# Kernel tuning notes

Hardware: AMD Instinct MI355X
Metric: run time of the kernel (lower is better)

## Reference

```python
import jax, jax.numpy as jnp
import numpy as np

N_NODES = 100000
N_EDGES = 1600000
IN_DIM, HID_DIM, OUT_DIM = 128, 128, 64


def setup_inputs() -> dict:
    key = jax.random.key(0)
    k1, k2, k3, k4 = jax.random.split(key, 4)
    x = jax.random.normal(k1, (N_NODES, IN_DIM), dtype=jnp.float32)
    edge_index = jax.random.randint(k2, (2, N_EDGES), 0, N_NODES, dtype=jnp.int64)
    W1 = jax.random.normal(k3, (IN_DIM, HID_DIM), dtype=jnp.float32) * (1.0 / np.sqrt(IN_DIM))
    b1 = jnp.zeros((HID_DIM,), dtype=jnp.float32)
    W2 = jax.random.normal(k4, (HID_DIM, OUT_DIM), dtype=jnp.float32) * (1.0 / np.sqrt(HID_DIM))
    b2 = jnp.zeros((OUT_DIM,), dtype=jnp.float32)
    return {"x": x, "edge_index": edge_index, "W1": W1, "b1": b1, "W2": W2, "b2": b2}


def _gcn_conv(h, src, dst, norm, W, b, n_nodes):
    # Dense transform first (PyG GCNConv order), then gather-scatter aggregation.
    h = h @ W                                   # [N, out]
    msg = h[src] * norm[:, None]                # [E, out] gather + scale
    out = jax.ops.segment_sum(msg, dst, num_segments=n_nodes)  # scatter-add
    return out + b


def reference(x, edge_index, W1, b1, W2, b2):
    src, dst = edge_index[0], edge_index[1]
    n = x.shape[0]
    # symmetric normalization: deg from in-degree (unit edge weights), no self loops
    deg = jax.ops.segment_sum(jnp.ones_like(src, dtype=x.dtype), dst, num_segments=n)
    deg_inv_sqrt = jnp.where(deg > 0, jax.lax.rsqrt(jnp.maximum(deg, 1.0)), 0.0)
    norm = deg_inv_sqrt[src] * deg_inv_sqrt[dst]  # [E]
    h = jax.nn.relu(_gcn_conv(x, src, dst, norm, W1, b1, n))
    # dropout is identity in eval mode
    out = _gcn_conv(h, src, dst, norm, W2, b2, n)
    return out
```

## Files before the change

kernel.cpp:

```cpp
#include <hip/hip_runtime.h>
#include <stdint.h>

#define NN 100000
#define NE 1600000
#define K_DIM 128

#define BSH 7
#define NBKT ((NN + (1 << BSH) - 1) >> BSH)
#define EPT 32
#define BIN_CHUNK (256 * EPT)
#define CAP 4096
#define PADE 2400000

typedef unsigned int uint32;
typedef unsigned short ushort16;
typedef __attribute__((ext_vector_type(8))) short bf16x8;
typedef __attribute__((ext_vector_type(4))) float f32x4;

__device__ __forceinline__ ushort16 f2bf(float f) {
    uint32 u = __float_as_uint(f);
    u += 0x7fffu + ((u >> 16) & 1u);
    return (ushort16)(u >> 16);
}
__device__ __forceinline__ float bf_lo(uint32 u) { return __uint_as_float(u << 16); }
__device__ __forceinline__ float bf_hi(uint32 u) { return __uint_as_float(u & 0xffff0000u); }

#define ACC8(v) do { \
    a0 += bf_lo((v).x); a1 += bf_hi((v).x); \
    a2 += bf_lo((v).y); a3 += bf_hi((v).y); \
    a4 += bf_lo((v).z); a5 += bf_hi((v).z); \
    a6 += bf_lo((v).w); a7 += bf_hi((v).w); } while (0)

__device__ __forceinline__ bf16x8 ld_frag8(const ushort16* p) {
    uint2 lo = *(const uint2*)p;
    uint2 hi = *(const uint2*)(p + 4);
    union { uint32 u[4]; bf16x8 v; } x;
    x.u[0] = lo.x; x.u[1] = lo.y; x.u[2] = hi.x; x.u[3] = hi.y;
    return x.v;
}


__global__ __launch_bounds__(256) void bin_pass1_kernel(
        const int* __restrict__ ei, int* __restrict__ gcursor,
        uint2* __restrict__ staging) {
    __shared__ int hist[NBKT];
    __shared__ int base[NBKT];
    int tid = threadIdx.x;
    int e0 = blockIdx.x * BIN_CHUNK;

    for (int i = tid; i < NBKT; i += 256) hist[i] = 0;
    __syncthreads();

    #pragma unroll
    for (int k = 0; k < EPT; k++) {
        int e = e0 + k * 256 + tid;
        if (e < NE) {
            int d = ei[NE + e];
            atomicAdd(&hist[d >> BSH], 1);
        }
    }
    __syncthreads();

    for (int i = tid; i < NBKT; i += 256) {
        int c = hist[i];
        base[i] = c ? atomicAdd(&gcursor[i], c) : 0;
        hist[i] = 0;
    }
    __syncthreads();

    #pragma unroll
    for (int k = 0; k < EPT; k++) {
        int e = e0 + k * 256 + tid;
        if (e < NE) {
            int s = ei[e];
            int d = ei[NE + e];
            int b = d >> BSH;
            int off = atomicAdd(&hist[b], 1);
            staging[(size_t)b * CAP + base[b] + off] = make_uint2((uint32)s, (uint32)d);
        }
    }
}

__global__ __launch_bounds__(256) void deg_bucket_kernel(
        const uint2* __restrict__ staging, const int* __restrict__ gcursor,
        int* __restrict__ deg, float* __restrict__ dis, int* __restrict__ bucket_tot) {
    __shared__ int cnt[1 << BSH];
    __shared__ int red[1 << BSH];
    int b = blockIdx.x;
    int node0 = b << BSH;
    int tid = threadIdx.x;
    int n_edges = gcursor[b];

    if (tid < (1 << BSH)) cnt[tid] = 0;
    __syncthreads();

    for (int i = tid; i < n_edges; i += 256) {
        uint2 p = staging[(size_t)b * CAP + i];
        atomicAdd(&cnt[p.y & ((1 << BSH) - 1)], 1);
    }
    __syncthreads();

    if (tid < (1 << BSH)) {
        int node = node0 + tid;
        int c = cnt[tid];
        if (node < NN) {
            deg[node] = c;
            dis[node] = (c > 0) ? rsqrtf((float)c) : 0.0f;
            red[tid] = (c + 7) & ~7;
        } else {
            red[tid] = 0;
        }
    }
    __syncthreads();
    for (int off = (1 << BSH) / 2; off > 0; off >>= 1) {
        if (tid < off) red[tid] += red[tid + off];
        __syncthreads();
    }
    if (tid == 0) bucket_tot[b] = red[0];
}

__global__ void bucket_scan_kernel(const int* __restrict__ bucket_tot,
                                   int* __restrict__ bucket_base,
                                   int* __restrict__ row_start) {
    __shared__ int buf[1024];
    int tid = threadIdx.x;
    int v = (tid < NBKT) ? bucket_tot[tid] : 0;
    buf[tid] = v;
    __syncthreads();
    for (int off = 1; off < 1024; off <<= 1) {
        int t = (tid >= off) ? buf[tid - off] : 0;
        __syncthreads();
        buf[tid] += t;
        __syncthreads();
    }
    if (tid < NBKT) bucket_base[tid] = buf[tid] - v;
    if (tid == NBKT - 1) row_start[NN] = buf[tid];
}

__global__ __launch_bounds__(256) void bin_pass2_kernel(
        const uint2* __restrict__ staging, const int* __restrict__ gcursor,
        const int* __restrict__ deg, const int* __restrict__ bucket_base,
        int* __restrict__ row_start, int* __restrict__ ssrc) {
    __shared__ int sb[1 << BSH];
    __shared__ int cur[1 << BSH];
    __shared__ int pend[1 << BSH];
    int b = blockIdx.x;
    int node0 = b << BSH;
    int tid = threadIdx.x;
    int n_edges = gcursor[b];

    int p = 0;
    if (tid < (1 << BSH)) {
        int node = node0 + tid;
        p = (node < NN) ? ((deg[node] + 7) & ~7) : 0;
        sb[tid] = p;
    }
    __syncthreads();
    #pragma unroll
    for (int off = 1; off < (1 << BSH); off <<= 1) {
        int t = (tid >= off && tid < (1 << BSH)) ? sb[tid - off] : 0;
        __syncthreads();
        if (tid < (1 << BSH)) sb[tid] += t;
        __syncthreads();
    }
    if (tid < (1 << BSH)) {
        int rs = bucket_base[b] + sb[tid] - p;
        cur[tid] = rs;
        pend[tid] = rs + p;
        int node = node0 + tid;
        if (node < NN) row_start[node] = rs;
    }
    __syncthreads();

    for (int i = tid; i < n_edges; i += 256) {
        uint2 pr = staging[(size_t)b * CAP + i];
        int off = atomicAdd(&cur[pr.y & ((1 << BSH) - 1)], 1);
        ssrc[off] = (int)pr.x;
    }
    __syncthreads();

    if (tid < (1 << BSH)) {
        int node = node0 + tid;
        if (node < NN) {
            for (int q = cur[tid]; q < pend[tid]; q++) ssrc[q] = NN;
        }
    }
}

template <int N, bool ABF16>
__global__ __launch_bounds__(256) void gemm_mfma_kernel(
        const void* __restrict__ Ap, const float* __restrict__ W,
        const float* __restrict__ dis, ushort16* __restrict__ out, int M) {
    constexpr int BM = 64, K = K_DIM;
    constexpr int LDA = 132;
    constexpr int NT = N / 16;
    constexpr int NLOG = (N == 128) ? 7 : 6;

    __shared__ ushort16 As[BM * LDA];
    __shared__ ushort16 Bt[N * LDA];

    int tid = threadIdx.x;
    int row0 = blockIdx.x * BM;

    if constexpr (!ABF16) {
        const float* A = (const float*)Ap;
        #pragma unroll
        for (int c = 0; c < 8; c++) {
            int idx = c * 1024 + tid * 4;
            int r = idx >> 7, col = idx & 127;
            int ra = row0 + r;
            float4 v = (ra < M) ? *(const float4*)&A[(size_t)ra * K + col]
                                : make_float4(0.f, 0.f, 0.f, 0.f);
            ushort4 bq;
            bq.x = f2bf(v.x); bq.y = f2bf(v.y); bq.z = f2bf(v.z); bq.w = f2bf(v.w);
            *(ushort4*)&As[r * LDA + col] = bq;
        }
    } else {
        const ushort16* A = (const ushort16*)Ap;
        #pragma unroll
        for (int c = 0; c < 4; c++) {
            int idx = c * 2048 + tid * 8;
            int r = idx >> 7, col = idx & 127;
            int ra = row0 + r;
            uint4 v = make_uint4(0u, 0u, 0u, 0u);
            if (ra < M) v = *(const uint4*)&A[(size_t)ra * K + col];
            *(uint2*)&As[r * LDA + col]     = make_uint2(v.x, v.y);
            *(uint2*)&As[r * LDA + col + 4] = make_uint2(v.z, v.w);
        }
    }
    {
        #pragma unroll
        for (int c = 0; c < (K * N) / 1024; c++) {
            int idx = c * 1024 + tid * 4;
            int k = idx >> NLOG, n = idx & (N - 1);
            float4 v = *(const float4*)&W[idx];
            Bt[(n + 0) * LDA + k] = f2bf(v.x);
            Bt[(n + 1) * LDA + k] = f2bf(v.y);
            Bt[(n + 2) * LDA + k] = f2bf(v.z);
            Bt[(n + 3) * LDA + k] = f2bf(v.w);
        }
    }
    __syncthreads();

    int lane = tid & 63;
    int wv = tid >> 6;
    int m0 = wv * 16;
    int ml = lane & 15;
    int quad = lane >> 4;

    f32x4 acc[NT];
    #pragma unroll
    for (int i = 0; i < NT; i++) acc[i] = (f32x4){0.f, 0.f, 0.f, 0.f};

    #pragma unroll
    for (int ks = 0; ks < 4; ks++) {
        int kof = ks * 32 + quad * 8;
        bf16x8 a = ld_frag8(&As[(m0 + ml) * LDA + kof]);
        #pragma unroll
        for (int nt = 0; nt < NT; nt++) {
            bf16x8 bb = ld_frag8(&Bt[(nt * 16 + ml) * LDA + kof]);
            acc[nt] = __builtin_amdgcn_mfma_f32_16x16x32_bf16(a, bb, acc[nt], 0, 0, 0);
        }
    }

    #pragma unroll
    for (int r = 0; r < 4; r++) {
        int row = row0 + m0 + quad * 4 + r;
        if (row < M) {
            float s = dis[row];
            #pragma unroll
            for (int nt = 0; nt < NT; nt++)
                out[(size_t)row * N + nt * 16 + ml] = f2bf(acc[nt][r] * s);
        }
    }
}

__global__ __launch_bounds__(256) void agg128_kernel(
        const ushort16* __restrict__ g, const int* __restrict__ row_start,
        const int* __restrict__ ssrc, const float* __restrict__ dis,
        const float* __restrict__ bias, ushort16* __restrict__ out) {
    int wave = (blockIdx.x * 256 + threadIdx.x) >> 6;
    int lane = threadIdx.x & 63;
    if (wave >= NN) return;

    int beg = row_start[wave];
    int end = row_start[wave + 1];
    int ecount = end - beg;
    float sc = dis[wave];

    int fl = lane & 15;
    int q  = lane >> 4;
    int laneoff = fl * 16;

    int idx = ssrc[beg + lane];

    float a0 = 0.f, a1 = 0.f, a2 = 0.f, a3 = 0.f;
    float a4 = 0.f, a5 = 0.f, a6 = 0.f, a7 = 0.f;

    const char* gb = (const char*)g;
    int nb = ((ecount < 64) ? ecount : 64) >> 3;
    int b = 0;
    for (; b + 2 <= nb; b += 2) {
        int s0a = __shfl(idx, b * 8 + q);
        int s1a = __shfl(idx, b * 8 + 4 + q);
        int s0b = __shfl(idx, b * 8 + 8 + q);
        int s1b = __shfl(idx, b * 8 + 12 + q);
        uint4 v0a = *(const uint4*)(gb + (((uint32)s0a << 8) + laneoff));
        uint4 v1a = *(const uint4*)(gb + (((uint32)s1a << 8) + laneoff));
        uint4 v0b = *(const uint4*)(gb + (((uint32)s0b << 8) + laneoff));
        uint4 v1b = *(const uint4*)(gb + (((uint32)s1b << 8) + laneoff));
        ACC8(v0a); ACC8(v1a); ACC8(v0b); ACC8(v1b);
    }
    if (b < nb) {
        int s0 = __shfl(idx, b * 8 + q);
        int s1 = __shfl(idx, b * 8 + 4 + q);
        uint4 v0 = *(const uint4*)(gb + (((uint32)s0 << 8) + laneoff));
        uint4 v1 = *(const uint4*)(gb + (((uint32)s1 << 8) + laneoff));
        ACC8(v0); ACC8(v1);
    }
    for (int e = beg + 64; e < end; e += 8) {
        int idx2 = ssrc[e + (lane & 7)];
        int s0 = __shfl(idx2, q);
        int s1 = __shfl(idx2, 4 + q);
        uint4 v0 = *(const uint4*)(gb + (((uint32)s0 << 8) + laneoff));
        uint4 v1 = *(const uint4*)(gb + (((uint32)s1 << 8) + laneoff));
        ACC8(v0); ACC8(v1);
    }

    a0 += __shfl_xor(a0, 16); a1 += __shfl_xor(a1, 16);
    a2 += __shfl_xor(a2, 16); a3 += __shfl_xor(a3, 16);
    a4 += __shfl_xor(a4, 16); a5 += __shfl_xor(a5, 16);
    a6 += __shfl_xor(a6, 16); a7 += __shfl_xor(a7, 16);
    a0 += __shfl_xor(a0, 32); a1 += __shfl_xor(a1, 32);
    a2 += __shfl_xor(a2, 32); a3 += __shfl_xor(a3, 32);
    a4 += __shfl_xor(a4, 32); a5 += __shfl_xor(a5, 32);
    a6 += __shfl_xor(a6, 32); a7 += __shfl_xor(a7, 32);

    if (lane < 16) {
        float4 bA = *(const float4*)&bias[fl * 8];
        float4 bB = *(const float4*)&bias[fl * 8 + 4];
        float o0 = fmaxf(sc * a0 + bA.x, 0.f);
        float o1 = fmaxf(sc * a1 + bA.y, 0.f);
        float o2 = fmaxf(sc * a2 + bA.z, 0.f);
        float o3 = fmaxf(sc * a3 + bA.w, 0.f);
        float o4 = fmaxf(sc * a4 + bB.x, 0.f);
        float o5 = fmaxf(sc * a5 + bB.y, 0.f);
        float o6 = fmaxf(sc * a6 + bB.z, 0.f);
        float o7 = fmaxf(sc * a7 + bB.w, 0.f);
        uint4 pk;
        pk.x = ((uint32)f2bf(o1) << 16) | (uint32)f2bf(o0);
        pk.y = ((uint32)f2bf(o3) << 16) | (uint32)f2bf(o2);
        pk.z = ((uint32)f2bf(o5) << 16) | (uint32)f2bf(o4);
        pk.w = ((uint32)f2bf(o7) << 16) | (uint32)f2bf(o6);
        *(uint4*)&out[(size_t)wave * 128 + fl * 8] = pk;
    }
}

__global__ __launch_bounds__(256) void agg64_kernel(
        const ushort16* __restrict__ g, const int* __restrict__ row_start,
        const int* __restrict__ ssrc, const float* __restrict__ dis,
        const float* __restrict__ bias, float* __restrict__ out) {
    int wave = (blockIdx.x * 256 + threadIdx.x) >> 6;
    int lane = threadIdx.x & 63;
    int half = lane >> 5;
    int l2 = lane & 31;
    int node = wave * 2 + half;
    if (node >= NN) return;

    int beg = row_start[node];
    int end = row_start[node + 1];
    int ecount = end - beg;
    float sc = dis[node];

    int fl = l2 & 7;
    int q  = l2 >> 3;
    int laneoff = fl * 16;

    int idx = ssrc[beg + l2];

    float a0 = 0.f, a1 = 0.f, a2 = 0.f, a3 = 0.f;
    float a4 = 0.f, a5 = 0.f, a6 = 0.f, a7 = 0.f;

    const char* gb = (const char*)g;
    int nb = ((ecount < 32) ? ecount : 32) >> 3;
    int b = 0;
    for (; b + 2 <= nb; b += 2) {
        int s0a = __shfl(idx, half * 32 + b * 8 + q);
        int s1a = __shfl(idx, half * 32 + b * 8 + 4 + q);
        int s0b = __shfl(idx, half * 32 + b * 8 + 8 + q);
        int s1b = __shfl(idx, half * 32 + b * 8 + 12 + q);
        uint4 v0a = *(const uint4*)(gb + (((uint32)s0a << 7) + laneoff));
        uint4 v1a = *(const uint4*)(gb + (((uint32)s1a << 7) + laneoff));
        uint4 v0b = *(const uint4*)(gb + (((uint32)s0b << 7) + laneoff));
        uint4 v1b = *(const uint4*)(gb + (((uint32)s1b << 7) + laneoff));
        ACC8(v0a); ACC8(v1a); ACC8(v0b); ACC8(v1b);
    }
    if (b < nb) {
        int s0 = __shfl(idx, half * 32 + b * 8 + q);
        int s1 = __shfl(idx, half * 32 + b * 8 + 4 + q);
        uint4 v0 = *(const uint4*)(gb + (((uint32)s0 << 7) + laneoff));
        uint4 v1 = *(const uint4*)(gb + (((uint32)s1 << 7) + laneoff));
        ACC8(v0); ACC8(v1);
    }
    for (int e = beg + 32; e < end; e += 8) {
        int idx2 = ssrc[e + (l2 & 7)];
        int s0 = __shfl(idx2, half * 32 + q);
        int s1 = __shfl(idx2, half * 32 + 4 + q);
        uint4 v0 = *(const uint4*)(gb + (((uint32)s0 << 7) + laneoff));
        uint4 v1 = *(const uint4*)(gb + (((uint32)s1 << 7) + laneoff));
        ACC8(v0); ACC8(v1);
    }

    a0 += __shfl_xor(a0, 8);  a1 += __shfl_xor(a1, 8);
    a2 += __shfl_xor(a2, 8);  a3 += __shfl_xor(a3, 8);
    a4 += __shfl_xor(a4, 8);  a5 += __shfl_xor(a5, 8);
    a6 += __shfl_xor(a6, 8);  a7 += __shfl_xor(a7, 8);
    a0 += __shfl_xor(a0, 16); a1 += __shfl_xor(a1, 16);
    a2 += __shfl_xor(a2, 16); a3 += __shfl_xor(a3, 16);
    a4 += __shfl_xor(a4, 16); a5 += __shfl_xor(a5, 16);
    a6 += __shfl_xor(a6, 16); a7 += __shfl_xor(a7, 16);

    if (l2 < 8) {
        float4 bA = *(const float4*)&bias[fl * 8];
        float4 bB = *(const float4*)&bias[fl * 8 + 4];
        float4 oA = make_float4(sc * a0 + bA.x, sc * a1 + bA.y,
                                sc * a2 + bA.z, sc * a3 + bA.w);
        float4 oB = make_float4(sc * a4 + bB.x, sc * a5 + bB.y,
                                sc * a6 + bB.z, sc * a7 + bB.w);
        *(float4*)&out[(size_t)node * 64 + fl * 8]     = oA;
        *(float4*)&out[(size_t)node * 64 + fl * 8 + 4] = oB;
    }
}

extern "C" void kernel_launch(void* const* d_in, const int* in_sizes, int n_in,
                              void* d_out, int out_size, void* d_ws, size_t ws_size,
                              hipStream_t stream) {
    const float* x  = (const float*)d_in[0];
    const int*   ei = (const int*)d_in[1];
    const float* W1 = (const float*)d_in[2];
    const float* b1 = (const float*)d_in[3];
    const float* W2 = (const float*)d_in[4];
    const float* b2 = (const float*)d_in[5];
    float* out = (float*)d_out;

    char* ws = (char*)d_ws;
    size_t off = 0;
    auto alloc = [&](size_t bytes) {
        void* p = ws + off;
        off = (off + bytes + 255) & ~(size_t)255;
        return p;
    };

    int*      deg_i      = (int*)alloc(NN * 4);
    float*    dis        = (float*)alloc(NN * 4);
    int*      row_start  = (int*)alloc((NN + 1) * 4);
    int*      gcursor    = (int*)alloc(NBKT * 4);
    int*      bucket_tot = (int*)alloc(NBKT * 4);
    int*      bucket_bse = (int*)alloc(NBKT * 4);
    int*      ssrc       = (int*)alloc((size_t)PADE * 4);
    ushort16* g1         = (ushort16*)alloc((size_t)(NN + 1) * 128 * 2);
    char*     big        = (char*)alloc((size_t)NBKT * CAP * 8);
    uint2*    staging    = (uint2*)big;
    ushort16* h          = (ushort16*)big;
    ushort16* g2         = g1;

    hipMemsetAsync(gcursor, 0, NBKT * 4, stream);
    hipMemsetAsync((char*)g1 + (size_t)NN * 256, 0, 256, stream);

    bin_pass1_kernel<<<(NE + BIN_CHUNK - 1) / BIN_CHUNK, 256, 0, stream>>>(ei, gcursor, staging);
    deg_bucket_kernel<<<NBKT, 256, 0, stream>>>(staging, gcursor, deg_i, dis, bucket_tot);
    bucket_scan_kernel<<<1, 1024, 0, stream>>>(bucket_tot, bucket_bse, row_start);
    bin_pass2_kernel<<<NBKT, 256, 0, stream>>>(staging, gcursor, deg_i, bucket_bse, row_start, ssrc);

    const int GEMM_BLOCKS = (NN + 63) / 64;
    gemm_mfma_kernel<128, false><<<GEMM_BLOCKS, 256, 0, stream>>>(x, W1, dis, g1, NN);

    const int AGG_BLOCKS = (NN + 3) / 4;
    agg128_kernel<<<AGG_BLOCKS, 256, 0, stream>>>(g1, row_start, ssrc, dis, b1, h);

    hipMemsetAsync((char*)g2 + (size_t)NN * 128, 0, 128, stream);

    gemm_mfma_kernel<64, true><<<GEMM_BLOCKS, 256, 0, stream>>>(h, W2, dis, g2, NN);

    const int AGG2_BLOCKS = (NN / 2 + 3) / 4;
    agg64_kernel<<<AGG2_BLOCKS, 256, 0, stream>>>(g2, row_start, ssrc, dis, b2, out);
}
```

Before: 275.4 us.

## Slice layer-1 features into column slabs for cache-resident gather aggregation

The first GEMM now writes its output as eight column slabs of 16 bf16 features each, 32 bytes per node per slab, instead of 256-byte rows. A new sliced aggregation kernel handles one slab per block, interleaved so consecutive blocks cover different slices. Each lane group gathers 4-byte words over neighbour indices from its slab. The goal is for each slab (about 3.2 MB) to stay resident in L2 or the MALL, so the random gathers hit cache instead of HBM. The cost is eight passes over the edge lists, more index loads, narrow 4-byte gathers, and per-wave loops sized to the maximum degree across the wave's 8 nodes.

```diff
diff --git a/kernel.cpp b/kernel.cpp
--- a/kernel.cpp
+++ b/kernel.cpp
@@ -11,6 +11,9 @@
 #define BIN_CHUNK (256 * EPT)
 #define CAP 4096
 #define PADE 2400000
+
+#define NSLICE 8
+#define SLAB1E ((NN + 1) * 16)
 
 typedef unsigned int uint32;
 typedef unsigned short ushort16;
@@ -187,7 +190,7 @@
     }
 }
 
-template <int N, bool ABF16>
+template <int N, bool ABF16, bool SLICED>
 __global__ __launch_bounds__(256) void gemm_mfma_kernel(
         const void* __restrict__ Ap, const float* __restrict__ W,
         const float* __restrict__ dis, ushort16* __restrict__ out, int M) {
@@ -201,6 +204,13 @@
 
     int tid = threadIdx.x;
     int row0 = blockIdx.x * BM;
+
+    if constexpr (SLICED) {
+        if (blockIdx.x == 0 && tid < 64) {
+            int sI = tid >> 3, cp = (tid & 7) * 2;
+            *(uint32*)&out[(size_t)sI * SLAB1E + (size_t)NN * 16 + cp] = 0u;
+        }
+    }
 
     if constexpr (!ABF16) {
         const float* A = (const float*)Ap;
@@ -269,91 +279,61 @@
         if (row < M) {
             float s = dis[row];
             #pragma unroll
-            for (int nt = 0; nt < NT; nt++)
-                out[(size_t)row * N + nt * 16 + ml] = f2bf(acc[nt][r] * s);
-        }
-    }
-}
-
-__global__ __launch_bounds__(256) void agg128_kernel(
+            for (int nt = 0; nt < NT; nt++) {
+                if constexpr (SLICED) {
+                    out[(size_t)nt * SLAB1E + (size_t)row * 16 + ml] = f2bf(acc[nt][r] * s);
+                } else {
+                    out[(size_t)row * N + nt * 16 + ml] = f2bf(acc[nt][r] * s);
+                }
+            }
+        }
+    }
+}
+
+__global__ __launch_bounds__(256) void agg128s_kernel(
         const ushort16* __restrict__ g, const int* __restrict__ row_start,
         const int* __restrict__ ssrc, const float* __restrict__ dis,
-        const float* __restrict__ bias, ushort16* __restrict__ out) {
-    int wave = (blockIdx.x * 256 + threadIdx.x) >> 6;
-    int lane = threadIdx.x & 63;
-    if (wave >= NN) return;
-
-    int beg = row_start[wave];
-    int end = row_start[wave + 1];
-    int ecount = end - beg;
-    float sc = dis[wave];
-
-    int fl = lane & 15;
-    int q  = lane >> 4;
-    int laneoff = fl * 16;
-
-    int idx = ssrc[beg + lane];
-
-    float a0 = 0.f, a1 = 0.f, a2 = 0.f, a3 = 0.f;
-    float a4 = 0.f, a5 = 0.f, a6 = 0.f, a7 = 0.f;
-
-    const char* gb = (const char*)g;
-    int nb = ((ecount < 64) ? ecount : 64) >> 3;
-    int b = 0;
-    for (; b + 2 <= nb; b += 2) {
-        int s0a = __shfl(idx, b * 8 + q);
-        int s1a = __shfl(idx, b * 8 + 4 + q);
-        int s0b = __shfl(idx, b * 8 + 8 + q);
-        int s1b = __shfl(idx, b * 8 + 12 + q);
-        uint4 v0a = *(const uint4*)(gb + (((uint32)s0a << 8) + laneoff));
-        uint4 v1a = *(const uint4*)(gb + (((uint32)s1a << 8) + laneoff));
-        uint4 v0b = *(const uint4*)(gb + (((uint32)s0b << 8) + laneoff));
-        uint4 v1b = *(const uint4*)(gb + (((uint32)s1b << 8) + laneoff));
-        ACC8(v0a); ACC8(v1a); ACC8(v0b); ACC8(v1b);
-    }
-    if (b < nb) {
-        int s0 = __shfl(idx, b * 8 + q);
-        int s1 = __shfl(idx, b * 8 + 4 + q);
-        uint4 v0 = *(const uint4*)(gb + (((uint32)s0 << 8) + laneoff));
-        uint4 v1 = *(const uint4*)(gb + (((uint32)s1 << 8) + laneoff));
-        ACC8(v0); ACC8(v1);
-    }
-    for (int e = beg + 64; e < end; e += 8) {
-        int idx2 = ssrc[e + (lane & 7)];
-        int s0 = __shfl(idx2, q);
-        int s1 = __shfl(idx2, 4 + q);
-        uint4 v0 = *(const uint4*)(gb + (((uint32)s0 << 8) + laneoff));
-        uint4 v1 = *(const uint4*)(gb + (((uint32)s1 << 8) + laneoff));
-        ACC8(v0); ACC8(v1);
-    }
-
-    a0 += __shfl_xor(a0, 16); a1 += __shfl_xor(a1, 16);
-    a2 += __shfl_xor(a2, 16); a3 += __shfl_xor(a3, 16);
-    a4 += __shfl_xor(a4, 16); a5 += __shfl_xor(a5, 16);
-    a6 += __shfl_xor(a6, 16); a7 += __shfl_xor(a7, 16);
-    a0 += __shfl_xor(a0, 32); a1 += __shfl_xor(a1, 32);
-    a2 += __shfl_xor(a2, 32); a3 += __shfl_xor(a3, 32);
-    a4 += __shfl_xor(a4, 32); a5 += __shfl_xor(a5, 32);
-    a6 += __shfl_xor(a6, 32); a7 += __shfl_xor(a7, 32);
-
-    if (lane < 16) {
-        float4 bA = *(const float4*)&bias[fl * 8];
-        float4 bB = *(const float4*)&bias[fl * 8 + 4];
-        float o0 = fmaxf(sc * a0 + bA.x, 0.f);
-        float o1 = fmaxf(sc * a1 + bA.y, 0.f);
-        float o2 = fmaxf(sc * a2 + bA.z, 0.f);
-        float o3 = fmaxf(sc * a3 + bA.w, 0.f);
-        float o4 = fmaxf(sc * a4 + bB.x, 0.f);
-        float o5 = fmaxf(sc * a5 + bB.y, 0.f);
-        float o6 = fmaxf(sc * a6 + bB.z, 0.f);
-        float o7 = fmaxf(sc * a7 + bB.w, 0.f);
-        uint4 pk;
-        pk.x = ((uint32)f2bf(o1) << 16) | (uint32)f2bf(o0);
-        pk.y = ((uint32)f2bf(o3) << 16) | (uint32)f2bf(o2);
-        pk.z = ((uint32)f2bf(o5) << 16) | (uint32)f2bf(o4);
-        pk.w = ((uint32)f2bf(o7) << 16) | (uint32)f2bf(o6);
-        *(uint4*)&out[(size_t)wave * 128 + fl * 8] = pk;
-    }
+        const float* __restrict__ bias, ushort16* __restrict__ h) {
+    int b = blockIdx.x;
+    int s = b & (NSLICE - 1);
+    int chunk = b >> 3;
+    int tid = threadIdx.x;
+    int wv = tid >> 6, lane = tid & 63;
+    int g8 = lane >> 3, fl = lane & 7;
+    int node = chunk * 32 + wv * 8 + g8;
+
+    int beg = row_start[node];
+    int end = row_start[node + 1];
+    int pdeg = end - beg;
+    float sc = dis[node];
+
+    int mx = pdeg;
+    mx = max(mx, __shfl_xor(mx, 8));
+    mx = max(mx, __shfl_xor(mx, 16));
+    mx = max(mx, __shfl_xor(mx, 32));
+
+    const char* slab = (const char*)g + (size_t)s * SLAB1E * 2;
+    uint32 colb = (uint32)fl * 4;
+
+    float a0 = 0.f, a1 = 0.f;
+
+    for (int k = 0; k < mx; k += 8) {
+        int e = k + fl;
+        int idxv = (e < pdeg) ? ssrc[beg + e] : NN;
+        #pragma unroll
+        for (int j = 0; j < 8; j++) {
+            int sidx = __shfl(idxv, g8 * 8 + j);
+            uint32 u = *(const uint32*)(slab + ((uint32)sidx * 32 + colb));
+            a0 += bf_lo(u);
+            a1 += bf_hi(u);
+        }
+    }
+
+    float2 bb = *(const float2*)&bias[s * 16 + fl * 2];
+    float o0 = fmaxf(sc * a0 + bb.x, 0.f);
+    float o1 = fmaxf(sc * a1 + bb.y, 0.f);
+    uint32 pk = ((uint32)f2bf(o1) << 16) | (uint32)f2bf(o0);
+    *(uint32*)((char*)h + ((size_t)node * 256 + s * 32 + fl * 4)) = pk;
 }
 
 __global__ __launch_bounds__(256) void agg64_kernel(
@@ -465,7 +445,6 @@
     ushort16* g2         = g1;
 
     hipMemsetAsync(gcursor, 0, NBKT * 4, stream);
-    hipMemsetAsync((char*)g1 + (size_t)NN * 256, 0, 256, stream);
 
     bin_pass1_kernel<<<(NE + BIN_CHUNK - 1) / BIN_CHUNK, 256, 0, stream>>>(ei, gcursor, staging);
     deg_bucket_kernel<<<NBKT, 256, 0, stream>>>(staging, gcursor, deg_i, dis, bucket_tot);
@@ -473,14 +452,14 @@
     bin_pass2_kernel<<<NBKT, 256, 0, stream>>>(staging, gcursor, deg_i, bucket_bse, row_start, ssrc);
 
     const int GEMM_BLOCKS = (NN + 63) / 64;
-    gemm_mfma_kernel<128, false><<<GEMM_BLOCKS, 256, 0, stream>>>(x, W1, dis, g1, NN);
-
-    const int AGG_BLOCKS = (NN + 3) / 4;
-    agg128_kernel<<<AGG_BLOCKS, 256, 0, stream>>>(g1, row_start, ssrc, dis, b1, h);
+    gemm_mfma_kernel<128, false, true><<<GEMM_BLOCKS, 256, 0, stream>>>(x, W1, dis, g1, NN);
+
+    const int AGG1_BLOCKS = (NN / 32) * NSLICE;
+    agg128s_kernel<<<AGG1_BLOCKS, 256, 0, stream>>>(g1, row_start, ssrc, dis, b1, h);
 
     hipMemsetAsync((char*)g2 + (size_t)NN * 128, 0, 128, stream);
 
-    gemm_mfma_kernel<64, true><<<GEMM_BLOCKS, 256, 0, stream>>>(h, W2, dis, g2, NN);
+    gemm_mfma_kernel<64, true, false><<<GEMM_BLOCKS, 256, 0, stream>>>(h, W2, dis, g2, NN);
 
     const int AGG2_BLOCKS = (NN / 2 + 3) / 4;
     agg64_kernel<<<AGG2_BLOCKS, 256, 0, stream>>>(g2, row_start, ssrc, dis, b2, out);
```

Result: slower. 306.5 us (+11.3%).

## Merge CSR build into one bucket kernel with atomic base allocation

Applied to the files above, without the earlier changes.

Packs each staged edge into one 32-bit word (src<<7 | local dst) instead of a uint2, which halves staging traffic. The degree, bucket-scan and pass2 kernels are merged into a single bucket_finish kernel: it caches the edges in LDS and claims its output region with one global atomicAdd instead of a separate scan. The aggregators now derive edge counts from deg rather than row_start[n+1], and the pad-row zeroing memsets move into the GEMM kernels. Together these remove several launches and memsets, at the cost of bucket placement in ssrc no longer following bucket order.

```diff
diff --git a/kernel.cpp b/kernel.cpp
--- a/kernel.cpp
+++ b/kernel.cpp
@@ -10,7 +10,7 @@
 #define EPT 32
 #define BIN_CHUNK (256 * EPT)
 #define CAP 4096
-#define PADE 2400000
+#define PADE 2301000
 
 typedef unsigned int uint32;
 typedef unsigned short ushort16;
@@ -42,7 +42,7 @@
 
 __global__ __launch_bounds__(256) void bin_pass1_kernel(
         const int* __restrict__ ei, int* __restrict__ gcursor,
-        uint2* __restrict__ staging) {
+        uint32* __restrict__ staging) {
     __shared__ int hist[NBKT];
     __shared__ int base[NBKT];
     int tid = threadIdx.x;
@@ -76,16 +76,22 @@
             int d = ei[NE + e];
             int b = d >> BSH;
             int off = atomicAdd(&hist[b], 1);
-            staging[(size_t)b * CAP + base[b] + off] = make_uint2((uint32)s, (uint32)d);
-        }
-    }
-}
-
-__global__ __launch_bounds__(256) void deg_bucket_kernel(
-        const uint2* __restrict__ staging, const int* __restrict__ gcursor,
-        int* __restrict__ deg, float* __restrict__ dis, int* __restrict__ bucket_tot) {
+            staging[(size_t)b * CAP + base[b] + off] =
+                ((uint32)s << 7) | (uint32)(d & 127);
+        }
+    }
+}
+
+__global__ __launch_bounds__(256) void bucket_finish_kernel(
+        const uint32* __restrict__ staging, const int* __restrict__ gcursor,
+        int* __restrict__ gedge, int* __restrict__ deg, float* __restrict__ dis,
+        int* __restrict__ row_start, int* __restrict__ ssrc) {
+    __shared__ uint32 pairs[CAP];
     __shared__ int cnt[1 << BSH];
-    __shared__ int red[1 << BSH];
+    __shared__ int sb[1 << BSH];
+    __shared__ int cur[1 << BSH];
+    __shared__ int pend[1 << BSH];
+    __shared__ int bbase;
     int b = blockIdx.x;
     int node0 = b << BSH;
     int tid = threadIdx.x;
@@ -95,64 +101,21 @@
     __syncthreads();
 
     for (int i = tid; i < n_edges; i += 256) {
-        uint2 p = staging[(size_t)b * CAP + i];
-        atomicAdd(&cnt[p.y & ((1 << BSH) - 1)], 1);
-    }
-    __syncthreads();
-
+        uint32 p = staging[(size_t)b * CAP + i];
+        pairs[i] = p;
+        atomicAdd(&cnt[p & 127u], 1);
+    }
+    __syncthreads();
+
+    int p = 0;
     if (tid < (1 << BSH)) {
         int node = node0 + tid;
         int c = cnt[tid];
         if (node < NN) {
             deg[node] = c;
             dis[node] = (c > 0) ? rsqrtf((float)c) : 0.0f;
-            red[tid] = (c + 7) & ~7;
-        } else {
-            red[tid] = 0;
-        }
-    }
-    __syncthreads();
-    for (int off = (1 << BSH) / 2; off > 0; off >>= 1) {
-        if (tid < off) red[tid] += red[tid + off];
-        __syncthreads();
-    }
-    if (tid == 0) bucket_tot[b] = red[0];
-}
-
-__global__ void bucket_scan_kernel(const int* __restrict__ bucket_tot,
-                                   int* __restrict__ bucket_base,
-                                   int* __restrict__ row_start) {
-    __shared__ int buf[1024];
-    int tid = threadIdx.x;
-    int v = (tid < NBKT) ? bucket_tot[tid] : 0;
-    buf[tid] = v;
-    __syncthreads();
-    for (int off = 1; off < 1024; off <<= 1) {
-        int t = (tid >= off) ? buf[tid - off] : 0;
-        __syncthreads();
-        buf[tid] += t;
-        __syncthreads();
-    }
-    if (tid < NBKT) bucket_base[tid] = buf[tid] - v;
-    if (tid == NBKT - 1) row_start[NN] = buf[tid];
-}
-
-__global__ __launch_bounds__(256) void bin_pass2_kernel(
-        const uint2* __restrict__ staging, const int* __restrict__ gcursor,
-        const int* __restrict__ deg, const int* __restrict__ bucket_base,
-        int* __restrict__ row_start, int* __restrict__ ssrc) {
-    __shared__ int sb[1 << BSH];
-    __shared__ int cur[1 << BSH];
-    __shared__ int pend[1 << BSH];
-    int b = blockIdx.x;
-    int node0 = b << BSH;
-    int tid = threadIdx.x;
-    int n_edges = gcursor[b];
-
-    int p = 0;
-    if (tid < (1 << BSH)) {
-        int node = node0 + tid;
-        p = (node < NN) ? ((deg[node] + 7) & ~7) : 0;
+            p = (c + 7) & ~7;
+        }
         sb[tid] = p;
     }
     __syncthreads();
@@ -163,8 +126,11 @@
         if (tid < (1 << BSH)) sb[tid] += t;
         __syncthreads();
     }
+    if (tid == (1 << BSH) - 1) bbase = atomicAdd(gedge, sb[tid]);
+    __syncthreads();
+
     if (tid < (1 << BSH)) {
-        int rs = bucket_base[b] + sb[tid] - p;
+        int rs = bbase + sb[tid] - p;
         cur[tid] = rs;
         pend[tid] = rs + p;
         int node = node0 + tid;
@@ -173,9 +139,9 @@
     __syncthreads();
 
     for (int i = tid; i < n_edges; i += 256) {
-        uint2 pr = staging[(size_t)b * CAP + i];
-        int off = atomicAdd(&cur[pr.y & ((1 << BSH) - 1)], 1);
-        ssrc[off] = (int)pr.x;
+        uint32 pr = pairs[i];
+        int off = atomicAdd(&cur[pr & 127u], 1);
+        ssrc[off] = (int)(pr >> 7);
     }
     __syncthreads();
 
@@ -187,7 +153,7 @@
     }
 }
 
-template <int N, bool ABF16>
+template <int N, bool ABF16, int ZROWB>
 __global__ __launch_bounds__(256) void gemm_mfma_kernel(
         const void* __restrict__ Ap, const float* __restrict__ W,
         const float* __restrict__ dis, ushort16* __restrict__ out, int M) {
@@ -201,6 +167,11 @@
 
     int tid = threadIdx.x;
     int row0 = blockIdx.x * BM;
+
+    if constexpr (ZROWB > 0) {
+        if (blockIdx.x == 0 && tid < ZROWB / 4)
+            ((uint32*)&out[(size_t)NN * N])[tid] = 0u;
+    }
 
     if constexpr (!ABF16) {
         const float* A = (const float*)Ap;
@@ -277,15 +248,15 @@
 
 __global__ __launch_bounds__(256) void agg128_kernel(
         const ushort16* __restrict__ g, const int* __restrict__ row_start,
-        const int* __restrict__ ssrc, const float* __restrict__ dis,
-        const float* __restrict__ bias, ushort16* __restrict__ out) {
+        const int* __restrict__ deg, const int* __restrict__ ssrc,
+        const float* __restrict__ dis, const float* __restrict__ bias,
+        ushort16* __restrict__ out) {
     int wave = (blockIdx.x * 256 + threadIdx.x) >> 6;
     int lane = threadIdx.x & 63;
     if (wave >= NN) return;
 
     int beg = row_start[wave];
-    int end = row_start[wave + 1];
-    int ecount = end - beg;
+    int ecount = (deg[wave] + 7) & ~7;
     float sc = dis[wave];
 
     int fl = lane & 15;
@@ -318,7 +289,7 @@
         uint4 v1 = *(const uint4*)(gb + (((uint32)s1 << 8) + laneoff));
         ACC8(v0); ACC8(v1);
     }
-    for (int e = beg + 64; e < end; e += 8) {
+    for (int e = beg + 64; e < beg + ecount; e += 8) {
         int idx2 = ssrc[e + (lane & 7)];
         int s0 = __shfl(idx2, q);
         int s1 = __shfl(idx2, 4 + q);
@@ -358,8 +329,9 @@
 
 __global__ __launch_bounds__(256) void agg64_kernel(
         const ushort16* __restrict__ g, const int* __restrict__ row_start,
-        const int* __restrict__ ssrc, const float* __restrict__ dis,
-        const float* __restrict__ bias, float* __restrict__ out) {
+        const int* __restrict__ deg, const int* __restrict__ ssrc,
+        const float* __restrict__ dis, const float* __restrict__ bias,
+        float* __restrict__ out) {
     int wave = (blockIdx.x * 256 + threadIdx.x) >> 6;
     int lane = threadIdx.x & 63;
     int half = lane >> 5;
@@ -368,8 +340,7 @@
     if (node >= NN) return;
 
     int beg = row_start[node];
-    int end = row_start[node + 1];
-    int ecount = end - beg;
+    int ecount = (deg[node] + 7) & ~7;
     float sc = dis[node];
 
     int fl = l2 & 7;
@@ -402,7 +373,7 @@
         uint4 v1 = *(const uint4*)(gb + (((uint32)s1 << 7) + laneoff));
         ACC8(v0); ACC8(v1);
     }
-    for (int e = beg + 32; e < end; e += 8) {
+    for (int e = beg + 32; e < beg + ecount; e += 8) {
         int idx2 = ssrc[e + (l2 & 7)];
         int s0 = __shfl(idx2, half * 32 + q);
         int s1 = __shfl(idx2, half * 32 + 4 + q);
@@ -453,35 +424,30 @@
 
     int*      deg_i      = (int*)alloc(NN * 4);
     float*    dis        = (float*)alloc(NN * 4);
-    int*      row_start  = (int*)alloc((NN + 1) * 4);
-    int*      gcursor    = (int*)alloc(NBKT * 4);
-    int*      bucket_tot = (int*)alloc(NBKT * 4);
-    int*      bucket_bse = (int*)alloc(NBKT * 4);
+    int*      row_start  = (int*)alloc(NN * 4);
+    int*      gcursor    = (int*)alloc((NBKT + 1) * 4);
     int*      ssrc       = (int*)alloc((size_t)PADE * 4);
     ushort16* g1         = (ushort16*)alloc((size_t)(NN + 1) * 128 * 2);
-    char*     big        = (char*)alloc((size_t)NBKT * CAP * 8);
-    uint2*    staging    = (uint2*)big;
-    ushort16* h          = (ushort16*)big;
+    ushort16* h          = (ushort16*)alloc((size_t)NN * 128 * 2);
+    uint32*   staging    = (uint32*)g1;
     ushort16* g2         = g1;
-
-    hipMemsetAsync(gcursor, 0, NBKT * 4, stream);
-    hipMemsetAsync((char*)g1 + (size_t)NN * 256, 0, 256, stream);
-
-    bin_pass1_kernel<<<(NE + BIN_CHUNK - 1) / BIN_CHUNK, 256, 0, stream>>>(ei, gcursor, staging);
-    deg_bucket_kernel<<<NBKT, 256, 0, stream>>>(staging, gcursor, deg_i, dis, bucket_tot);
-    bucket_scan_kernel<<<1, 1024, 0, stream>>>(bucket_tot, bucket_bse, row_start);
-    bin_pass2_kernel<<<NBKT, 256, 0, stream>>>(staging, gcursor, deg_i, bucket_bse, row_start, ssrc);
+    int*      gedge      = gcursor + NBKT;
+
+    hipMemsetAsync(gcursor, 0, (NBKT + 1) * 4, stream);
+
+    bin_pass1_kernel<<<(NE + BIN_CHUNK - 1) / BIN_CHUNK, 256, 0, stream>>>(
+        ei, gcursor, staging);
+    bucket_finish_kernel<<<NBKT, 256, 0, stream>>>(
+        staging, gcursor, gedge, deg_i, dis, row_start, ssrc);
 
     const int GEMM_BLOCKS = (NN + 63) / 64;
-    gemm_mfma_kernel<128, false><<<GEMM_BLOCKS, 256, 0, stream>>>(x, W1, dis, g1, NN);
+    gemm_mfma_kernel<128, false, 256><<<GEMM_BLOCKS, 256, 0, stream>>>(x, W1, dis, g1, NN);
 
     const int AGG_BLOCKS = (NN + 3) / 4;
-    agg128_kernel<<<AGG_BLOCKS, 256, 0, stream>>>(g1, row_start, ssrc, dis, b1, h);
-
-    hipMemsetAsync((char*)g2 + (size_t)NN * 128, 0, 128, stream);
-
-    gemm_mfma_kernel<64, true><<<GEMM_BLOCKS, 256, 0, stream>>>(h, W2, dis, g2, NN);
+    agg128_kernel<<<AGG_BLOCKS, 256, 0, stream>>>(g1, row_start, deg_i, ssrc, dis, b1, h);
+
+    gemm_mfma_kernel<64, true, 128><<<GEMM_BLOCKS, 256, 0, stream>>>(h, W2, dis, g2, NN);
 
     const int AGG2_BLOCKS = (NN / 2 + 3) / 4;
-    agg64_kernel<<<AGG2_BLOCKS, 256, 0, stream>>>(g2, row_start, ssrc, dis, b2, out);
-}
+    agg64_kernel<<<AGG2_BLOCKS, 256, 0, stream>>>(g2, row_start, deg_i, ssrc, dis, b2, out);
+}
```

Measured after the change: 281.9 us. 2.4% more time.
